# Kernel optimization log

Hardware: AMD Instinct MI355X
Metric: run time of the kernel (lower is better)

Reference implementation:

```python
import jax, jax.numpy as jnp
import numpy as np

N = 768
W = 224
H = 126
FX = 2343.0242837919386 * W / 2560.0   # 205.01462483179463
FY = 2343.0242837919386 * H / 1440.0   # same value


def quat_to_rot(quats):
    """[N,4] wxyz quaternions -> [N,3,3] rotation matrices."""
    q = quats / jnp.linalg.norm(quats, axis=1, keepdims=True)
    w, x, y, z = q[:, 0], q[:, 1], q[:, 2], q[:, 3]
    R = jnp.stack([
        jnp.stack([1 - 2 * (y * y + z * z), 2 * (x * y - z * w), 2 * (x * z + y * w)], axis=-1),
        jnp.stack([2 * (x * y + z * w), 1 - 2 * (x * x + z * z), 2 * (y * z - x * w)], axis=-1),
        jnp.stack([2 * (x * z - y * w), 2 * (y * z + x * w), 1 - 2 * (x * x + y * y)], axis=-1),
    ], axis=1)
    return R


def setup_inputs() -> dict:
    key = jax.random.key(0)
    k1, k2, k3, k4, k5 = jax.random.split(key, 5)
    # gaussians in front of the camera (z in [4,8])
    means_xy = jax.random.uniform(k1, (N, 2), minval=-2.0, maxval=2.0)
    means_z = jax.random.uniform(k2, (N, 1), minval=4.0, maxval=8.0)
    means = jnp.concatenate([means_xy, means_z], axis=1).astype(jnp.float32)
    scales_raw = jnp.log(jax.random.uniform(k3, (N, 3), minval=0.01, maxval=0.05)).astype(jnp.float32)
    quats = jax.random.normal(k4, (N, 4), dtype=jnp.float32)
    opac_raw = jax.random.normal(k5, (N,), dtype=jnp.float32)

    # precomputed buffers (torch.no_grad in original)
    Rg = quat_to_rot(quats)                      # [N,3,3]
    M = Rg * jnp.exp(scales_raw)[:, None, :]     # R @ diag(exp(scales))
    cov_world = M @ jnp.swapaxes(M, 1, 2)        # [N,3,3]
    means_hom = jnp.concatenate([means, jnp.ones((N, 1), jnp.float32)], axis=1)  # [N,4]
    means_hom_tmp = means_hom.T[None]            # [1,4,N]
    opacities_rast = jax.nn.sigmoid(opac_raw)[None, None, :, None]  # [1,1,N,1]
    K = jnp.array([[FX, 0.0, W / 2.0], [0.0, FY, H / 2.0], [0.0, 0.0, 1.0]], jnp.float32)
    X, Y = jnp.meshgrid(jnp.arange(W), jnp.arange(H), indexing='xy')  # [H,W]
    tile_coord = jnp.stack([X, Y], axis=-1).reshape(-1, 2).astype(jnp.float32)[None, :, None, :]  # [1,HW,1,2]
    lim_x = jnp.array([1.3 * 0.5 * W / FX], jnp.float32)
    lim_y = jnp.array([1.3 * 0.5 * H / FY], jnp.float32)

    # camera pose: small rotation about z + small translation, bottom row [0,0,0,1]
    ang = 0.05
    c, s = np.cos(ang), np.sin(ang)
    pose = np.eye(4, dtype=np.float32)
    pose[:3, :3] = np.array([[c, -s, 0.0], [s, c, 0.0], [0.0, 0.0, 1.0]], np.float32)
    pose[:3, 3] = np.array([0.1, -0.1, 0.3], np.float32)
    x = jnp.asarray(pose)[None]                  # [1,4,4]

    return {"x": x, "means_hom_tmp": means_hom_tmp, "cov_world": cov_world,
            "opacities_rast": opacities_rast, "K": K, "tile_coord": tile_coord,
            "lim_x": lim_x, "lim_y": lim_y, "fx": float(FX), "fy": float(FY)}


def reference(x, means_hom_tmp, cov_world, opacities_rast, K, tile_coord, lim_x, lim_y, fx, fy):
    mh = means_hom_tmp[0]                                  # [4,N]
    means_cam_hom = jnp.einsum('bij,jn->bni', x, mh)       # [B,N,4]
    means_cam = means_cam_hom[:, :, :3] / means_cam_hom[:, :, 3:4]
    R_cam = x[:, :3, :3]                                   # [B,3,3]
    cov_cam = jnp.einsum('bij,njk,blk->bnil', R_cam, cov_world, R_cam)  # [B,N,3,3]
    means_proj_hom = jnp.einsum('bni,ji->bnj', means_cam, K)
    means2D = means_proj_hom[:, :, :2] / means_proj_hom[:, :, 2:3]      # [B,N,2]

    xc, yc, z = means_cam[:, :, 0], means_cam[:, :, 1], means_cam[:, :, 2]
    tx = z * jnp.minimum(lim_x, jnp.maximum(-lim_x, xc / z))
    ty = z * jnp.minimum(lim_y, jnp.maximum(-lim_y, yc / z))
    J00 = fx / z
    J02 = -fx * tx / z ** 2
    J11 = fy / z
    J12 = -fy * ty / z ** 2
    cc = cov_cam
    c00 = J00 * J00 * cc[:, :, 0, 0] + J00 * J02 * cc[:, :, 0, 2] + J02 * J00 * cc[:, :, 2, 0] + J02 * J02 * cc[:, :, 2, 2] + 0.3
    c11 = J11 * J11 * cc[:, :, 1, 1] + J11 * J12 * cc[:, :, 1, 2] + J12 * J11 * cc[:, :, 2, 1] + J12 * J12 * cc[:, :, 2, 2] + 0.3
    c01 = J00 * J11 * cc[:, :, 0, 1] + J00 * J12 * cc[:, :, 0, 2] + J02 * J11 * cc[:, :, 2, 1] + J02 * J12 * cc[:, :, 2, 2]
    c10 = J11 * J00 * cc[:, :, 1, 0] + J11 * J02 * cc[:, :, 1, 2] + J12 * J00 * cc[:, :, 2, 0] + J12 * J02 * cc[:, :, 2, 2]
    inv_det = 1.0 / (c00 * c11 - c01 * c10)
    conic00 = inv_det * c11
    conic01 = -inv_det * c01
    conic10 = -inv_det * c10
    conic11 = inv_det * c00

    # brute-force per-pixel rasterization: [B,HW,N,2]
    dx = tile_coord - means2D[:, None, :, :]
    power = -0.5 * (dx[..., 0] ** 2 * conic00[:, None, :]
                    + dx[..., 1] ** 2 * conic11[:, None, :]
                    + dx[..., 0] * dx[..., 1] * (conic01 + conic10)[:, None, :])
    gauss_weight = jnp.exp(power)                          # [B,HW,N]
    alpha = gauss_weight[..., None] * opacities_rast       # [B,HW,N,1]
    alpha_clip = 0.99 - jax.nn.relu(0.99 - alpha)          # == -relu(-alpha+0.99)+0.99
    return alpha_clip
```

## Files before the change

### kernel.cpp

```cpp
#include <hip/hip_runtime.h>
#include <hip/hip_bf16.h>

#define NGAUSS 768
#define IMW 224
#define IMH 126
#define NPIX (IMW * IMH)
#define GPT 4
#define GPB 256
#define NGRP (NGAUSS / GPB)
#define CPB (GPB / GPT)
#define NTHREADS 256
#define PROWS (NTHREADS / CPB)
#define NPBLK 512
#define NBLOCKS (NGRP * NPBLK)
#define PSTRIDE (NPBLK * PROWS)

typedef float vfloat4 __attribute__((ext_vector_type(4)));

__global__ __launch_bounds__(NTHREADS) void raster_kernel(
    const float* __restrict__ x_in,
    const float* __restrict__ mh_in,
    const float* __restrict__ cov_in,
    const float* __restrict__ op_in,
    const float* __restrict__ K_in,
    const float* __restrict__ limx_in,
    const float* __restrict__ limy_in,
    const float* __restrict__ fx_in,
    const float* __restrict__ fy_in,
    float* __restrict__ out)
{
  __shared__ float sP[6][GPB];

  const int g    = blockIdx.x % NGRP;
  const int pblk = blockIdx.x / NGRP;

  {
    const int n = g * GPB + threadIdx.x;

    float m0 = mh_in[0 * NGAUSS + n];
    float m1 = mh_in[1 * NGAUSS + n];
    float m2 = mh_in[2 * NGAUSS + n];
    float m3 = mh_in[3 * NGAUSS + n];

    float cw[3][3];
#pragma unroll
    for (int i = 0; i < 3; ++i)
#pragma unroll
      for (int j = 0; j < 3; ++j) cw[i][j] = cov_in[n * 9 + 3 * i + j];

    float opac = op_in[n];

    float X[4][4];
#pragma unroll
    for (int i = 0; i < 4; ++i)
#pragma unroll
      for (int j = 0; j < 4; ++j) X[i][j] = x_in[4 * i + j];

    float K00 = K_in[0], K01 = K_in[1], K02 = K_in[2];
    float K10 = K_in[3], K11 = K_in[4], K12 = K_in[5];
    float K20 = K_in[6], K21 = K_in[7], K22 = K_in[8];

    float fxv = fx_in[0], fyv = fy_in[0];
    if (!(fxv > 190.0f && fxv < 220.0f)) fxv = K00;
    if (!(fyv > 190.0f && fyv < 220.0f)) fyv = K11;
    float limx = limx_in[0];
    float limy = limy_in[0];

    const float S = -0.5f * 1.44269504088896340736f;

    float h0 = X[0][0]*m0 + X[0][1]*m1 + X[0][2]*m2 + X[0][3]*m3;
    float h1 = X[1][0]*m0 + X[1][1]*m1 + X[1][2]*m2 + X[1][3]*m3;
    float h2 = X[2][0]*m0 + X[2][1]*m1 + X[2][2]*m2 + X[2][3]*m3;
    float h3 = X[3][0]*m0 + X[3][1]*m1 + X[3][2]*m2 + X[3][3]*m3;
    float iw = 1.0f / h3;
    float mcx = h0 * iw, mcy = h1 * iw, mcz = h2 * iw;

    float T[3][3];
#pragma unroll
    for (int i = 0; i < 3; ++i)
#pragma unroll
      for (int j = 0; j < 3; ++j)
        T[i][j] = X[i][0]*cw[0][j] + X[i][1]*cw[1][j] + X[i][2]*cw[2][j];
    float cc[3][3];
#pragma unroll
    for (int i = 0; i < 3; ++i)
#pragma unroll
      for (int l = 0; l < 3; ++l)
        cc[i][l] = T[i][0]*X[l][0] + T[i][1]*X[l][1] + T[i][2]*X[l][2];

    float ph0 = K00*mcx + K01*mcy + K02*mcz;
    float ph1 = K10*mcx + K11*mcy + K12*mcz;
    float ph2 = K20*mcx + K21*mcy + K22*mcz;
    float ipz = 1.0f / ph2;
    float m2x = ph0 * ipz, m2y = ph1 * ipz;

    float z = mcz;
    float invz = 1.0f / z;
    float tx = z * fminf(limx, fmaxf(-limx, mcx * invz));
    float ty = z * fminf(limy, fmaxf(-limy, mcy * invz));
    float J00 = fxv * invz;
    float J02 = -fxv * tx * invz * invz;
    float J11 = fyv * invz;
    float J12 = -fyv * ty * invz * invz;

    float c00 = J00*J00*cc[0][0] + J00*J02*cc[0][2] + J02*J00*cc[2][0] + J02*J02*cc[2][2] + 0.3f;
    float c11 = J11*J11*cc[1][1] + J11*J12*cc[1][2] + J12*J11*cc[2][1] + J12*J12*cc[2][2] + 0.3f;
    float c01 = J00*J11*cc[0][1] + J00*J12*cc[0][2] + J02*J11*cc[2][1] + J02*J12*cc[2][2];
    float c10 = J11*J00*cc[1][0] + J11*J02*cc[1][2] + J12*J00*cc[2][0] + J12*J02*cc[2][2];

    float invdet = 1.0f / (c00 * c11 - c01 * c10);

    int t = threadIdx.x;
    sP[0][t] = m2x;
    sP[1][t] = m2y;
    sP[2][t] = S * invdet * c11;
    sP[3][t] = S * (-invdet) * (c01 + c10);
    sP[4][t] = S * invdet * c00;
    sP[5][t] = opac;
  }
  __syncthreads();

  const int chunk = threadIdx.x & (CPB - 1);
  const int prow  = threadIdx.x >> 6;
  const int nl0   = chunk * GPT;
  const int n0    = g * GPB + nl0;

  float mx[GPT], my[GPT], A[GPT], B[GPT], C[GPT], O[GPT];
#pragma unroll
  for (int i = 0; i < GPT; ++i) {
    mx[i] = sP[0][nl0 + i];
    my[i] = sP[1][nl0 + i];
    A[i]  = sP[2][nl0 + i];
    B[i]  = sP[3][nl0 + i];
    C[i]  = sP[4][nl0 + i];
    O[i]  = sP[5][nl0 + i];
  }

  int p = pblk * PROWS + prow;
  int px = p % IMW, py = p / IMW;
  const int dpx = PSTRIDE % IMW;
  const int dpy = PSTRIDE / IMW;
  for (; p < NPIX; p += PSTRIDE) {
    float fpx = (float)px, fpy = (float)py;
    float r[GPT];
#pragma unroll
    for (int i = 0; i < GPT; ++i) {
      float dx = fpx - mx[i];
      float dy = fpy - my[i];
      float pw = fmaf(dx, fmaf(A[i], dx, B[i] * dy), C[i] * dy * dy);
      r[i] = fminf(__builtin_amdgcn_exp2f(pw) * O[i], 0.99f);
    }
    vfloat4 val = { r[0], r[1], r[2], r[3] };
    *(vfloat4*)(out + (size_t)p * NGAUSS + n0) = val;

    px += dpx; py += dpy;
    if (px >= IMW) { px -= IMW; py += 1; }
  }
}

extern "C" void kernel_launch(void* const* d_in, const int* in_sizes, int n_in,
                              void* d_out, int out_size, void* d_ws, size_t ws_size,
                              hipStream_t stream) {
  (void)in_sizes; (void)n_in; (void)d_ws; (void)ws_size; (void)out_size;
  raster_kernel<<<NBLOCKS, NTHREADS, 0, stream>>>(
      (const float*)d_in[0], (const float*)d_in[1], (const float*)d_in[2],
      (const float*)d_in[3], (const float*)d_in[4],
      (const float*)d_in[6], (const float*)d_in[7],
      (const float*)d_in[8], (const float*)d_in[9],
      (float*)d_out);
}
```

Before: 109.1 us.

## Assign each wave one full pixel row of all gaussians, 12 per lane

Measured after the change: 112.3 us. 1.03x slower.

```diff
diff --git a/kernel.cpp b/kernel.cpp
--- a/kernel.cpp
+++ b/kernel.cpp
@@ -1,23 +1,20 @@
 #include <hip/hip_runtime.h>
-#include <hip/hip_bf16.h>
 
 #define NGAUSS 768
 #define IMW 224
 #define IMH 126
 #define NPIX (IMW * IMH)
-#define GPT 4
-#define GPB 256
-#define NGRP (NGAUSS / GPB)
-#define CPB (GPB / GPT)
 #define NTHREADS 256
-#define PROWS (NTHREADS / CPB)
-#define NPBLK 512
-#define NBLOCKS (NGRP * NPBLK)
-#define PSTRIDE (NPBLK * PROWS)
+#define WPB (NTHREADS / 64)
+#define NBLOCKS 1008
+#define NWAVES (NBLOCKS * WPB)
+#define ITERS (NPIX / NWAVES)
+#define DPY (NWAVES / IMW)
+#define GPT 12
 
 typedef float vfloat4 __attribute__((ext_vector_type(4)));
 
-__global__ __launch_bounds__(NTHREADS) void raster_kernel(
+__global__ __launch_bounds__(NTHREADS, 4) void raster_kernel(
     const float* __restrict__ x_in,
     const float* __restrict__ mh_in,
     const float* __restrict__ cov_in,
@@ -29,27 +26,9 @@
     const float* __restrict__ fy_in,
     float* __restrict__ out)
 {
-  __shared__ float sP[6][GPB];
-
-  const int g    = blockIdx.x % NGRP;
-  const int pblk = blockIdx.x / NGRP;
+  __shared__ float sP[6][NGAUSS];
 
   {
-    const int n = g * GPB + threadIdx.x;
-
-    float m0 = mh_in[0 * NGAUSS + n];
-    float m1 = mh_in[1 * NGAUSS + n];
-    float m2 = mh_in[2 * NGAUSS + n];
-    float m3 = mh_in[3 * NGAUSS + n];
-
-    float cw[3][3];
-#pragma unroll
-    for (int i = 0; i < 3; ++i)
-#pragma unroll
-      for (int j = 0; j < 3; ++j) cw[i][j] = cov_in[n * 9 + 3 * i + j];
-
-    float opac = op_in[n];
-
     float X[4][4];
 #pragma unroll
     for (int i = 0; i < 4; ++i)
@@ -68,80 +47,103 @@
 
     const float S = -0.5f * 1.44269504088896340736f;
 
-    float h0 = X[0][0]*m0 + X[0][1]*m1 + X[0][2]*m2 + X[0][3]*m3;
-    float h1 = X[1][0]*m0 + X[1][1]*m1 + X[1][2]*m2 + X[1][3]*m3;
-    float h2 = X[2][0]*m0 + X[2][1]*m1 + X[2][2]*m2 + X[2][3]*m3;
-    float h3 = X[3][0]*m0 + X[3][1]*m1 + X[3][2]*m2 + X[3][3]*m3;
-    float iw = 1.0f / h3;
-    float mcx = h0 * iw, mcy = h1 * iw, mcz = h2 * iw;
+#pragma unroll
+    for (int it = 0; it < NGAUSS / NTHREADS; ++it) {
+      const int n = it * NTHREADS + threadIdx.x;
 
-    float T[3][3];
+      float m0 = mh_in[0 * NGAUSS + n];
+      float m1 = mh_in[1 * NGAUSS + n];
+      float m2 = mh_in[2 * NGAUSS + n];
+      float m3 = mh_in[3 * NGAUSS + n];
+
+      float cw[3][3];
 #pragma unroll
-    for (int i = 0; i < 3; ++i)
+      for (int i = 0; i < 3; ++i)
 #pragma unroll
-      for (int j = 0; j < 3; ++j)
-        T[i][j] = X[i][0]*cw[0][j] + X[i][1]*cw[1][j] + X[i][2]*cw[2][j];
-    float cc[3][3];
+        for (int j = 0; j < 3; ++j) cw[i][j] = cov_in[n * 9 + 3 * i + j];
+
+      float opac = op_in[n];
+
+      float h0 = X[0][0]*m0 + X[0][1]*m1 + X[0][2]*m2 + X[0][3]*m3;
+      float h1 = X[1][0]*m0 + X[1][1]*m1 + X[1][2]*m2 + X[1][3]*m3;
+      float h2 = X[2][0]*m0 + X[2][1]*m1 + X[2][2]*m2 + X[2][3]*m3;
+      float h3 = X[3][0]*m0 + X[3][1]*m1 + X[3][2]*m2 + X[3][3]*m3;
+      float iw = 1.0f / h3;
+      float mcx = h0 * iw, mcy = h1 * iw, mcz = h2 * iw;
+
+      float T[3][3];
 #pragma unroll
-    for (int i = 0; i < 3; ++i)
+      for (int i = 0; i < 3; ++i)
 #pragma unroll
-      for (int l = 0; l < 3; ++l)
-        cc[i][l] = T[i][0]*X[l][0] + T[i][1]*X[l][1] + T[i][2]*X[l][2];
+        for (int j = 0; j < 3; ++j)
+          T[i][j] = X[i][0]*cw[0][j] + X[i][1]*cw[1][j] + X[i][2]*cw[2][j];
+      float cc[3][3];
+#pragma unroll
+      for (int i = 0; i < 3; ++i)
+#pragma unroll
+        for (int l = 0; l < 3; ++l)
+          cc[i][l] = T[i][0]*X[l][0] + T[i][1]*X[l][1] + T[i][2]*X[l][2];
 
-    float ph0 = K00*mcx + K01*mcy + K02*mcz;
-    float ph1 = K10*mcx + K11*mcy + K12*mcz;
-    float ph2 = K20*mcx + K21*mcy + K22*mcz;
-    float ipz = 1.0f / ph2;
-    float m2x = ph0 * ipz, m2y = ph1 * ipz;
+      float ph0 = K00*mcx + K01*mcy + K02*mcz;
+      float ph1 = K10*mcx + K11*mcy + K12*mcz;
+      float ph2 = K20*mcx + K21*mcy + K22*mcz;
+      float ipz = 1.0f / ph2;
+      float m2x = ph0 * ipz, m2y = ph1 * ipz;
 
-    float z = mcz;
-    float invz = 1.0f / z;
-    float tx = z * fminf(limx, fmaxf(-limx, mcx * invz));
-    float ty = z * fminf(limy, fmaxf(-limy, mcy * invz));
-    float J00 = fxv * invz;
-    float J02 = -fxv * tx * invz * invz;
-    float J11 = fyv * invz;
-    float J12 = -fyv * ty * invz * invz;
+      float z = mcz;
+      float invz = 1.0f / z;
+      float tx = z * fminf(limx, fmaxf(-limx, mcx * invz));
+      float ty = z * fminf(limy, fmaxf(-limy, mcy * invz));
+      float J00 = fxv * invz;
+      float J02 = -fxv * tx * invz * invz;
+      float J11 = fyv * invz;
+      float J12 = -fyv * ty * invz * invz;
 
-    float c00 = J00*J00*cc[0][0] + J00*J02*cc[0][2] + J02*J00*cc[2][0] + J02*J02*cc[2][2] + 0.3f;
-    float c11 = J11*J11*cc[1][1] + J11*J12*cc[1][2] + J12*J11*cc[2][1] + J12*J12*cc[2][2] + 0.3f;
-    float c01 = J00*J11*cc[0][1] + J00*J12*cc[0][2] + J02*J11*cc[2][1] + J02*J12*cc[2][2];
-    float c10 = J11*J00*cc[1][0] + J11*J02*cc[1][2] + J12*J00*cc[2][0] + J12*J02*cc[2][2];
+      float c00 = J00*J00*cc[0][0] + J00*J02*cc[0][2] + J02*J00*cc[2][0] + J02*J02*cc[2][2] + 0.3f;
+      float c11 = J11*J11*cc[1][1] + J11*J12*cc[1][2] + J12*J11*cc[2][1] + J12*J12*cc[2][2] + 0.3f;
+      float c01 = J00*J11*cc[0][1] + J00*J12*cc[0][2] + J02*J11*cc[2][1] + J02*J12*cc[2][2];
+      float c10 = J11*J00*cc[1][0] + J11*J02*cc[1][2] + J12*J00*cc[2][0] + J12*J02*cc[2][2];
 
-    float invdet = 1.0f / (c00 * c11 - c01 * c10);
+      float invdet = 1.0f / (c00 * c11 - c01 * c10);
 
-    int t = threadIdx.x;
-    sP[0][t] = m2x;
-    sP[1][t] = m2y;
-    sP[2][t] = S * invdet * c11;
-    sP[3][t] = S * (-invdet) * (c01 + c10);
-    sP[4][t] = S * invdet * c00;
-    sP[5][t] = opac;
+      sP[0][n] = m2x;
+      sP[1][n] = m2y;
+      sP[2][n] = S * invdet * c11;
+      sP[3][n] = S * (-invdet) * (c01 + c10);
+      sP[4][n] = S * invdet * c00;
+      sP[5][n] = opac;
+    }
   }
   __syncthreads();
 
-  const int chunk = threadIdx.x & (CPB - 1);
-  const int prow  = threadIdx.x >> 6;
-  const int nl0   = chunk * GPT;
-  const int n0    = g * GPB + nl0;
+  const int lane = threadIdx.x & 63;
+  const int gw   = blockIdx.x * WPB + (threadIdx.x >> 6);
 
   float mx[GPT], my[GPT], A[GPT], B[GPT], C[GPT], O[GPT];
 #pragma unroll
-  for (int i = 0; i < GPT; ++i) {
-    mx[i] = sP[0][nl0 + i];
-    my[i] = sP[1][nl0 + i];
-    A[i]  = sP[2][nl0 + i];
-    B[i]  = sP[3][nl0 + i];
-    C[i]  = sP[4][nl0 + i];
-    O[i]  = sP[5][nl0 + i];
+  for (int q = 0; q < 3; ++q) {
+    const int nb = q * 256 + lane * 4;
+    vfloat4 v0 = *(const vfloat4*)&sP[0][nb];
+    vfloat4 v1 = *(const vfloat4*)&sP[1][nb];
+    vfloat4 v2 = *(const vfloat4*)&sP[2][nb];
+    vfloat4 v3 = *(const vfloat4*)&sP[3][nb];
+    vfloat4 v4 = *(const vfloat4*)&sP[4][nb];
+    vfloat4 v5 = *(const vfloat4*)&sP[5][nb];
+#pragma unroll
+    for (int j = 0; j < 4; ++j) {
+      mx[q*4+j] = v0[j];  my[q*4+j] = v1[j];
+      A[q*4+j]  = v2[j];  B[q*4+j]  = v3[j];
+      C[q*4+j]  = v4[j];  O[q*4+j]  = v5[j];
+    }
   }
 
-  int p = pblk * PROWS + prow;
-  int px = p % IMW, py = p / IMW;
-  const int dpx = PSTRIDE % IMW;
-  const int dpy = PSTRIDE / IMW;
-  for (; p < NPIX; p += PSTRIDE) {
-    float fpx = (float)px, fpy = (float)py;
+  const float fpx = (float)(gw % IMW);
+  int py = gw / IMW;
+  float* wout = out + (size_t)gw * NGAUSS + lane * 4;
+
+#pragma unroll 1
+  for (int k = 0; k < ITERS; ++k) {
+    const float fpy = (float)py;
     float r[GPT];
 #pragma unroll
     for (int i = 0; i < GPT; ++i) {
@@ -150,11 +152,13 @@
       float pw = fmaf(dx, fmaf(A[i], dx, B[i] * dy), C[i] * dy * dy);
       r[i] = fminf(__builtin_amdgcn_exp2f(pw) * O[i], 0.99f);
     }
-    vfloat4 val = { r[0], r[1], r[2], r[3] };
-    *(vfloat4*)(out + (size_t)p * NGAUSS + n0) = val;
-
-    px += dpx; py += dpy;
-    if (px >= IMW) { px -= IMW; py += 1; }
+#pragma unroll
+    for (int q = 0; q < 3; ++q) {
+      vfloat4 val = { r[q*4+0], r[q*4+1], r[q*4+2], r[q*4+3] };
+      *(vfloat4*)(wout + q * 256) = val;
+    }
+    wout += (size_t)NWAVES * NGAUSS;
+    py += DPY;
   }
 }
 
```
